# Kernel tuning notes

Measured on AMD Instinct MI355X. Metric: run time of the kernel, lower is better.

The kernel has to match this reference:

```python
import jax, jax.numpy as jnp
import numpy as np

B, A, D = 256, 32, 2048  # batch, num attributes, hidden_dim


def setup_inputs() -> dict:
    key = jax.random.key(0)
    k1, k2, k3, k4, k5 = jax.random.split(key, 5)
    x = jax.random.normal(k1, (B, D), dtype=jnp.float32)
    attribute_feat = jax.random.normal(k2, (B, A, D), dtype=jnp.float32)
    attribute_label = jax.random.randint(k3, (B, A), 0, 2, dtype=jnp.int64)
    # GraphConvolution parameters (glorot-style scale)
    W = jax.random.normal(k4, (D, D), dtype=jnp.float32) * (1.0 / np.sqrt(D))
    b = jnp.zeros((D,), dtype=jnp.float32)
    return {"x": x, "attribute_feat": attribute_feat,
            "attribute_label": attribute_label, "W": W, "b": b}


def reference(x, attribute_feat, attribute_label, W, b):
    # Star adjacency: nonzero attribute nodes <-> global node (index A)
    mask = (attribute_label > 0).astype(x.dtype)            # [B, A]
    adj = jnp.zeros((B, A + 1, A + 1), dtype=x.dtype)
    adj = adj.at[:, :A, A].set(mask).at[:, A, :A].set(mask)  # [B, A+1, A+1]
    # Vertex features: attributes + global node (x) per sample
    vertex = jnp.concatenate([attribute_feat, x[:, None, :]], axis=1)  # [B, A+1, D]
    # GCN layer: tanh(adj @ (vertex @ W) + b); dropout is identity in eval
    support = jnp.einsum('bnd,de->bne', vertex, W)           # [B, A+1, D]
    out = jnp.tanh(jnp.einsum('bnm,bmd->bnd', adj, support) + b)
    # Return updated global-node embedding per sample
    return out[:, -1, :]                                     # [B, D]
```

## Files before the change

kernel.cpp:

```cpp
#include <hip/hip_runtime.h>
#include <hip/hip_bf16.h>

typedef unsigned short ushort_t;
using ushort4v = __attribute__((ext_vector_type(4))) ushort_t;
using ushort8 = __attribute__((ext_vector_type(8))) ushort_t;
using short8  = __attribute__((ext_vector_type(8))) short;
using float4v = __attribute__((ext_vector_type(4))) float;

#define Bsz 256
#define Aattr 32
#define Ddim 2048
#define OUTN (Bsz * Ddim)

__device__ __forceinline__ float bf2f(ushort_t u) {
    union { unsigned int i; float f; } c;
    c.i = ((unsigned int)u) << 16;
    return c.f;
}

__device__ __forceinline__ ushort_t f2bf(float f) {
    union { float f; unsigned int i; } c;
    c.f = f;
    unsigned int x = c.i;
    unsigned int r = (x + 0x7FFFu + ((x >> 16) & 1u)) >> 16;
    return (ushort_t)r;
}

struct BfPair { ushort_t hi, lo; };
__device__ __forceinline__ BfPair split_bf16(float x) {
    BfPair p;
    p.hi = f2bf(x);
    p.lo = f2bf(x - bf2f(p.hi));
    return p;
}

__global__ __launch_bounds__(256) void k_prep(
    const float* __restrict__ feat, const int* __restrict__ label,
    const float* __restrict__ W,
    ushort_t* __restrict__ s_hi, ushort_t* __restrict__ s_lo,
    ushort_t* __restrict__ WT_hi, ushort_t* __restrict__ WT_lo) {
    __shared__ float tile[64][65];
    const int t = threadIdx.x;

    if (blockIdx.x < 512) {
        int* list = (int*)&tile[0][0];
        int* cntp = (int*)&tile[1][0];
        const int b    = blockIdx.x >> 1;
        const int half = blockIdx.x & 1;

        if (t < 64) {
            int lab = label[b * Aattr + (t & 31)];
            unsigned long long vote = __ballot(lab > 0);
            unsigned m32 = (unsigned)(vote & 0xFFFFFFFFull);
            if (t < 32) {
                if (lab > 0) {
                    int rank = __popc(m32 & ((1u << t) - 1u));
                    list[rank] = t;
                }
                if (t == 0) *cntp = __popc(m32);
            }
        }
        __syncthreads();

        const int n  = *cntp;
        const int d0 = half * 1024 + t * 4;
        const float* fb = feat + (size_t)b * (Aattr * Ddim) + d0;

        float a0 = 0.f, a1 = 0.f, a2 = 0.f, a3 = 0.f;
        int i = 0;
        for (; i + 4 <= n; i += 4) {
            const int j0 = list[i], j1 = list[i+1], j2 = list[i+2], j3 = list[i+3];
            float4 v0 = *(const float4*)(fb + j0 * Ddim);
            float4 v1 = *(const float4*)(fb + j1 * Ddim);
            float4 v2 = *(const float4*)(fb + j2 * Ddim);
            float4 v3 = *(const float4*)(fb + j3 * Ddim);
            a0 += v0.x + v1.x + v2.x + v3.x;
            a1 += v0.y + v1.y + v2.y + v3.y;
            a2 += v0.z + v1.z + v2.z + v3.z;
            a3 += v0.w + v1.w + v2.w + v3.w;
        }
        for (; i < n; ++i) {
            float4 v = *(const float4*)(fb + list[i] * Ddim);
            a0 += v.x; a1 += v.y; a2 += v.z; a3 += v.w;
        }

        ushort4v hi, lo;
        BfPair p0 = split_bf16(a0); hi[0] = p0.hi; lo[0] = p0.lo;
        BfPair p1 = split_bf16(a1); hi[1] = p1.hi; lo[1] = p1.lo;
        BfPair p2 = split_bf16(a2); hi[2] = p2.hi; lo[2] = p2.lo;
        BfPair p3 = split_bf16(a3); hi[3] = p3.hi; lo[3] = p3.lo;
        *(ushort4v*)(s_hi + (size_t)b * Ddim + d0) = hi;
        *(ushort4v*)(s_lo + (size_t)b * Ddim + d0) = lo;
    } else {
        const int q  = blockIdx.x - 512;
        const int bx = q & 31;
        const int by = q >> 5;

#pragma unroll
        for (int p = 0; p < 4; ++p) {
            const int row = p * 16 + (t >> 4);
            const int c   = (t & 15) * 4;
            float4 v = *(const float4*)(W + (size_t)(by * 64 + row) * Ddim + bx * 64 + c);
            tile[row][c + 0] = v.x;
            tile[row][c + 1] = v.y;
            tile[row][c + 2] = v.z;
            tile[row][c + 3] = v.w;
        }
        __syncthreads();
#pragma unroll
        for (int p = 0; p < 2; ++p) {
            const int er = p * 32 + (t >> 3);
            const int dc = (t & 7) * 8;
            ushort8 hi, lo;
#pragma unroll
            for (int j = 0; j < 8; ++j) {
                BfPair pr = split_bf16(tile[dc + j][er]);
                hi[j] = pr.hi; lo[j] = pr.lo;
            }
            const size_t off = (size_t)(bx * 64 + er) * Ddim + by * 64 + dc;
            *(ushort8*)(WT_hi + off) = hi;
            *(ushort8*)(WT_lo + off) = lo;
        }
    }
}

__global__ __launch_bounds__(64) void k_gemm(
    const ushort_t* __restrict__ S_hi, const ushort_t* __restrict__ S_lo,
    const ushort_t* __restrict__ WT_hi, const ushort_t* __restrict__ WT_lo,
    float* __restrict__ partials, int KS, int lks, int kchunk) {
    const int g    = blockIdx.x;
    const int ks   = g & (KS - 1);
    const int r    = g >> lks;
    const int m0   = (r & 3) * 64;
    const int n0   = (r >> 2) * 64;
    const int k0   = ks * kchunk;

    const int l    = threadIdx.x;
    const int quad = l >> 4;
    const int m16  = l & 15;

    float4v acc[4][4];
#pragma unroll
    for (int i = 0; i < 4; ++i)
#pragma unroll
        for (int j = 0; j < 4; ++j) acc[i][j] = {0.f, 0.f, 0.f, 0.f};

    const size_t aoff = (size_t)(m0 + m16) * Ddim + quad * 8;
    const size_t boff = (size_t)(n0 + m16) * Ddim + quad * 8;
    const ushort_t* Ah = S_hi + aoff;
    const ushort_t* Al = S_lo + aoff;
    const ushort_t* Bh = WT_hi + boff;
    const ushort_t* Bl = WT_lo + boff;

    for (int k = k0; k < k0 + kchunk; k += 32) {
        short8 ah[4], al[4], bh[4], bl[4];
#pragma unroll
        for (int i = 0; i < 4; ++i) {
            const size_t o = (size_t)(i * 16) * Ddim + k;
            ah[i] = *(const short8*)(Ah + o);
            al[i] = *(const short8*)(Al + o);
            bh[i] = *(const short8*)(Bh + o);
            bl[i] = *(const short8*)(Bl + o);
        }
#pragma unroll
        for (int mi = 0; mi < 4; ++mi) {
#pragma unroll
            for (int ni = 0; ni < 4; ++ni) {
                acc[mi][ni] = __builtin_amdgcn_mfma_f32_16x16x32_bf16(ah[mi], bh[ni], acc[mi][ni], 0, 0, 0);
                acc[mi][ni] = __builtin_amdgcn_mfma_f32_16x16x32_bf16(ah[mi], bl[ni], acc[mi][ni], 0, 0, 0);
                acc[mi][ni] = __builtin_amdgcn_mfma_f32_16x16x32_bf16(al[mi], bh[ni], acc[mi][ni], 0, 0, 0);
            }
        }
    }

    float* pout = partials + (size_t)ks * OUTN;
#pragma unroll
    for (int mi = 0; mi < 4; ++mi) {
#pragma unroll
        for (int ni = 0; ni < 4; ++ni) {
            const int n = n0 + ni * 16 + m16;
#pragma unroll
            for (int rr = 0; rr < 4; ++rr) {
                const int m = m0 + mi * 16 + quad * 4 + rr;
                pout[(size_t)m * Ddim + n] = acc[mi][ni][rr];
            }
        }
    }
}

__global__ __launch_bounds__(256) void k_finish(
    const float* __restrict__ partials, const float* __restrict__ bias,
    float* __restrict__ out, int KS) {
    const int i = (blockIdx.x * 256 + threadIdx.x) * 4;
    float a0 = 0.f, a1 = 0.f, a2 = 0.f, a3 = 0.f;
    for (int s = 0; s < KS; ++s) {
        float4 v = *(const float4*)(partials + (size_t)s * OUTN + i);
        a0 += v.x; a1 += v.y; a2 += v.z; a3 += v.w;
    }
    float4 bv = *(const float4*)(bias + (i & (Ddim - 1)));
    float4 o;
    o.x = tanhf(a0 + bv.x);
    o.y = tanhf(a1 + bv.y);
    o.z = tanhf(a2 + bv.z);
    o.w = tanhf(a3 + bv.w);
    *(float4*)(out + i) = o;
}

extern "C" void kernel_launch(void* const* d_in, const int* in_sizes, int n_in,
                              void* d_out, int out_size, void* d_ws, size_t ws_size,
                              hipStream_t stream) {
    const float* feat  = (const float*)d_in[1];
    const int*   label = (const int*)d_in[2];
    const float* W     = (const float*)d_in[3];
    const float* bias  = (const float*)d_in[4];
    float*       out   = (float*)d_out;

    char* ws = (char*)d_ws;
    ushort_t* s_hi  = (ushort_t*)ws;
    ushort_t* s_lo  = (ushort_t*)(ws + (1u << 20));
    ushort_t* WT_hi = (ushort_t*)(ws + (2u << 20));
    ushort_t* WT_lo = (ushort_t*)(ws + (10u << 20));
    float* partials = (float*)(ws + (18u << 20));

    const size_t avail = ws_size > (18u << 20) ? ws_size - (18u << 20) : 0;
    int KS = 1, lks = 0;
    while (KS < 8 && (size_t)(KS * 2) * (OUTN * sizeof(float)) <= avail) { KS *= 2; ++lks; }
    const int kchunk = Ddim / KS;

    k_prep<<<dim3(1536), dim3(256), 0, stream>>>(feat, label, W, s_hi, s_lo, WT_hi, WT_lo);
    k_gemm<<<dim3(128 * KS), dim3(64), 0, stream>>>(s_hi, s_lo, WT_hi, WT_lo,
                                                    partials, KS, lks, kchunk);
    k_finish<<<dim3(OUTN / 1024), dim3(256), 0, stream>>>(partials, bias, out, KS);
}
```

Baseline: 138.8 us.

## Fuse split-K reduction and tanh epilogue into GEMM via in-block LDS reduction

Replaces the split-K GEMM, which wrote per-split partials to global memory, and the separate finish kernel with one kernel. Each 256-thread block covers a 32x64 output tile, its four waves each take a quarter of K, and the partial sums are reduced through shared memory before bias and tanh are applied in place. This removes a kernel launch and the global round trip of up to 8 partial buffers. In exchange the grid shrinks to 256 blocks with smaller M tiles, which lowers B-operand reuse and may leave compute units underused.

Result: no change. 137.9 us (median of 2 runs) (-0.6%).

```diff
diff --git a/kernel.cpp b/kernel.cpp
--- a/kernel.cpp
+++ b/kernel.cpp
@@ -10,7 +10,6 @@
 #define Bsz 256
 #define Aattr 32
 #define Ddim 2048
-#define OUTN (Bsz * Ddim)
 
 __device__ __forceinline__ float bf2f(ushort_t u) {
     union { unsigned int i; float f; } c;
@@ -124,24 +123,28 @@
     }
 }
 
-__global__ __launch_bounds__(64) void k_gemm(
+__global__ __launch_bounds__(256) void k_gemm2(
     const ushort_t* __restrict__ S_hi, const ushort_t* __restrict__ S_lo,
     const ushort_t* __restrict__ WT_hi, const ushort_t* __restrict__ WT_lo,
-    float* __restrict__ partials, int KS, int lks, int kchunk) {
-    const int g    = blockIdx.x;
-    const int ks   = g & (KS - 1);
-    const int r    = g >> lks;
-    const int m0   = (r & 3) * 64;
-    const int n0   = (r >> 2) * 64;
-    const int k0   = ks * kchunk;
-
-    const int l    = threadIdx.x;
+    const float* __restrict__ bias, float* __restrict__ out) {
+    __shared__ float red[4][32 * 64];
+
+    const int g      = blockIdx.x;
+    const int n_tile = (g & 7) * 4 + (g >> 6);
+    const int m_tile = (g >> 3) & 7;
+    const int m0     = m_tile * 32;
+    const int n0     = n_tile * 64;
+
+    const int t    = threadIdx.x;
+    const int w    = t >> 6;
+    const int l    = t & 63;
     const int quad = l >> 4;
     const int m16  = l & 15;
-
-    float4v acc[4][4];
-#pragma unroll
-    for (int i = 0; i < 4; ++i)
+    const int k0   = w * 512;
+
+    float4v acc[2][4];
+#pragma unroll
+    for (int i = 0; i < 2; ++i)
 #pragma unroll
         for (int j = 0; j < 4; ++j) acc[i][j] = {0.f, 0.f, 0.f, 0.f};
 
@@ -152,58 +155,68 @@
     const ushort_t* Bh = WT_hi + boff;
     const ushort_t* Bl = WT_lo + boff;
 
-    for (int k = k0; k < k0 + kchunk; k += 32) {
-        short8 ah[4], al[4], bh[4], bl[4];
+    for (int k = k0; k < k0 + 512; k += 32) {
+        short8 ah0 = *(const short8*)(Ah + k);
+        short8 ah1 = *(const short8*)(Ah + 16 * Ddim + k);
+        short8 al0 = *(const short8*)(Al + k);
+        short8 al1 = *(const short8*)(Al + 16 * Ddim + k);
+        short8 bh[4], bl[4];
 #pragma unroll
         for (int i = 0; i < 4; ++i) {
             const size_t o = (size_t)(i * 16) * Ddim + k;
-            ah[i] = *(const short8*)(Ah + o);
-            al[i] = *(const short8*)(Al + o);
             bh[i] = *(const short8*)(Bh + o);
             bl[i] = *(const short8*)(Bl + o);
         }
 #pragma unroll
-        for (int mi = 0; mi < 4; ++mi) {
-#pragma unroll
-            for (int ni = 0; ni < 4; ++ni) {
-                acc[mi][ni] = __builtin_amdgcn_mfma_f32_16x16x32_bf16(ah[mi], bh[ni], acc[mi][ni], 0, 0, 0);
-                acc[mi][ni] = __builtin_amdgcn_mfma_f32_16x16x32_bf16(ah[mi], bl[ni], acc[mi][ni], 0, 0, 0);
-                acc[mi][ni] = __builtin_amdgcn_mfma_f32_16x16x32_bf16(al[mi], bh[ni], acc[mi][ni], 0, 0, 0);
+        for (int ni = 0; ni < 4; ++ni) {
+            acc[0][ni] = __builtin_amdgcn_mfma_f32_16x16x32_bf16(ah0, bh[ni], acc[0][ni], 0, 0, 0);
+            acc[0][ni] = __builtin_amdgcn_mfma_f32_16x16x32_bf16(ah0, bl[ni], acc[0][ni], 0, 0, 0);
+            acc[0][ni] = __builtin_amdgcn_mfma_f32_16x16x32_bf16(al0, bh[ni], acc[0][ni], 0, 0, 0);
+            acc[1][ni] = __builtin_amdgcn_mfma_f32_16x16x32_bf16(ah1, bh[ni], acc[1][ni], 0, 0, 0);
+            acc[1][ni] = __builtin_amdgcn_mfma_f32_16x16x32_bf16(ah1, bl[ni], acc[1][ni], 0, 0, 0);
+            acc[1][ni] = __builtin_amdgcn_mfma_f32_16x16x32_bf16(al1, bh[ni], acc[1][ni], 0, 0, 0);
+        }
+    }
+
+#pragma unroll
+    for (int mi = 0; mi < 2; ++mi) {
+#pragma unroll
+        for (int ni = 0; ni < 4; ++ni) {
+#pragma unroll
+            for (int rr = 0; rr < 4; ++rr) {
+                red[w][(mi * 16 + quad * 4 + rr) * 64 + ni * 16 + m16] = acc[mi][ni][rr];
             }
         }
     }
-
-    float* pout = partials + (size_t)ks * OUTN;
-#pragma unroll
-    for (int mi = 0; mi < 4; ++mi) {
-#pragma unroll
-        for (int ni = 0; ni < 4; ++ni) {
-            const int n = n0 + ni * 16 + m16;
-#pragma unroll
-            for (int rr = 0; rr < 4; ++rr) {
-                const int m = m0 + mi * 16 + quad * 4 + rr;
-                pout[(size_t)m * Ddim + n] = acc[mi][ni][rr];
-            }
-        }
-    }
-}
-
-__global__ __launch_bounds__(256) void k_finish(
-    const float* __restrict__ partials, const float* __restrict__ bias,
-    float* __restrict__ out, int KS) {
-    const int i = (blockIdx.x * 256 + threadIdx.x) * 4;
-    float a0 = 0.f, a1 = 0.f, a2 = 0.f, a3 = 0.f;
-    for (int s = 0; s < KS; ++s) {
-        float4 v = *(const float4*)(partials + (size_t)s * OUTN + i);
-        a0 += v.x; a1 += v.y; a2 += v.z; a3 += v.w;
-    }
-    float4 bv = *(const float4*)(bias + (i & (Ddim - 1)));
-    float4 o;
-    o.x = tanhf(a0 + bv.x);
-    o.y = tanhf(a1 + bv.y);
-    o.z = tanhf(a2 + bv.z);
-    o.w = tanhf(a3 + bv.w);
-    *(float4*)(out + i) = o;
+    __syncthreads();
+
+    const int m_l = t >> 3;
+    const int n_l = (t & 7) * 8;
+    const int base = m_l * 64 + n_l;
+    float s[8];
+#pragma unroll
+    for (int j = 0; j < 8; ++j) s[j] = 0.f;
+#pragma unroll
+    for (int ww = 0; ww < 4; ++ww) {
+        float4 v0 = *(const float4*)&red[ww][base];
+        float4 v1 = *(const float4*)&red[ww][base + 4];
+        s[0] += v0.x; s[1] += v0.y; s[2] += v0.z; s[3] += v0.w;
+        s[4] += v1.x; s[5] += v1.y; s[6] += v1.z; s[7] += v1.w;
+    }
+    float4 b0 = *(const float4*)(bias + n0 + n_l);
+    float4 b1 = *(const float4*)(bias + n0 + n_l + 4);
+    float4 o0, o1;
+    o0.x = tanhf(s[0] + b0.x);
+    o0.y = tanhf(s[1] + b0.y);
+    o0.z = tanhf(s[2] + b0.z);
+    o0.w = tanhf(s[3] + b0.w);
+    o1.x = tanhf(s[4] + b1.x);
+    o1.y = tanhf(s[5] + b1.y);
+    o1.z = tanhf(s[6] + b1.z);
+    o1.w = tanhf(s[7] + b1.w);
+    float* op = out + (size_t)(m0 + m_l) * Ddim + n0 + n_l;
+    *(float4*)op = o0;
+    *(float4*)(op + 4) = o1;
 }
 
 extern "C" void kernel_launch(void* const* d_in, const int* in_sizes, int n_in,
@@ -220,15 +233,7 @@
     ushort_t* s_lo  = (ushort_t*)(ws + (1u << 20));
     ushort_t* WT_hi = (ushort_t*)(ws + (2u << 20));
     ushort_t* WT_lo = (ushort_t*)(ws + (10u << 20));
-    float* partials = (float*)(ws + (18u << 20));
-
-    const size_t avail = ws_size > (18u << 20) ? ws_size - (18u << 20) : 0;
-    int KS = 1, lks = 0;
-    while (KS < 8 && (size_t)(KS * 2) * (OUTN * sizeof(float)) <= avail) { KS *= 2; ++lks; }
-    const int kchunk = Ddim / KS;
 
     k_prep<<<dim3(1536), dim3(256), 0, stream>>>(feat, label, W, s_hi, s_lo, WT_hi, WT_lo);
-    k_gemm<<<dim3(128 * KS), dim3(64), 0, stream>>>(s_hi, s_lo, WT_hi, WT_lo,
-                                                    partials, KS, lks, kchunk);
-    k_finish<<<dim3(OUTN / 1024), dim3(256), 0, stream>>>(partials, bias, out, KS);
-}
+    k_gemm2<<<dim3(256), dim3(256), 0, stream>>>(s_hi, s_lo, WT_hi, WT_lo, bias, out);
+}
```

## Fuse split-K reduction and tanh epilogue into GEMM via shared memory

Applied to the files above, without the earlier changes.

The GEMM now uses 256-thread blocks where each of four waves handles a quarter of K, reducing partial tiles in shared memory and applying bias plus tanh directly. This removes the global partials buffer round-trip and the separate finish kernel launch. In exchange the grid shrinks to 128 blocks, fewer than before when KS was 8, and the block tile order is remapped. It also uses 64KB of shared memory per block, which limits occupancy.

After: 147.9 us. 1.07x slower.

```diff
diff --git a/kernel.cpp b/kernel.cpp
--- a/kernel.cpp
+++ b/kernel.cpp
@@ -10,7 +10,6 @@
 #define Bsz 256
 #define Aattr 32
 #define Ddim 2048
-#define OUTN (Bsz * Ddim)
 
 __device__ __forceinline__ float bf2f(ushort_t u) {
     union { unsigned int i; float f; } c;
@@ -124,20 +123,24 @@
     }
 }
 
-__global__ __launch_bounds__(64) void k_gemm(
+__global__ __launch_bounds__(256) void k_gemm2(
     const ushort_t* __restrict__ S_hi, const ushort_t* __restrict__ S_lo,
     const ushort_t* __restrict__ WT_hi, const ushort_t* __restrict__ WT_lo,
-    float* __restrict__ partials, int KS, int lks, int kchunk) {
-    const int g    = blockIdx.x;
-    const int ks   = g & (KS - 1);
-    const int r    = g >> lks;
-    const int m0   = (r & 3) * 64;
-    const int n0   = (r >> 2) * 64;
-    const int k0   = ks * kchunk;
-
-    const int l    = threadIdx.x;
+    const float* __restrict__ bias, float* __restrict__ out) {
+    __shared__ float red[4][64 * 64];
+
+    const int g      = blockIdx.x;
+    const int n_tile = (g & 7) * 4 + (g >> 5);
+    const int m_tile = (g >> 3) & 3;
+    const int m0     = m_tile * 64;
+    const int n0     = n_tile * 64;
+
+    const int t    = threadIdx.x;
+    const int w    = t >> 6;
+    const int l    = t & 63;
     const int quad = l >> 4;
     const int m16  = l & 15;
+    const int k0   = w * 512;
 
     float4v acc[4][4];
 #pragma unroll
@@ -152,7 +155,8 @@
     const ushort_t* Bh = WT_hi + boff;
     const ushort_t* Bl = WT_lo + boff;
 
-    for (int k = k0; k < k0 + kchunk; k += 32) {
+#pragma unroll 2
+    for (int k = k0; k < k0 + 512; k += 32) {
         short8 ah[4], al[4], bh[4], bl[4];
 #pragma unroll
         for (int i = 0; i < 4; ++i) {
@@ -173,37 +177,35 @@
         }
     }
 
-    float* pout = partials + (size_t)ks * OUTN;
 #pragma unroll
     for (int mi = 0; mi < 4; ++mi) {
 #pragma unroll
         for (int ni = 0; ni < 4; ++ni) {
-            const int n = n0 + ni * 16 + m16;
 #pragma unroll
             for (int rr = 0; rr < 4; ++rr) {
-                const int m = m0 + mi * 16 + quad * 4 + rr;
-                pout[(size_t)m * Ddim + n] = acc[mi][ni][rr];
-            }
-        }
-    }
-}
-
-__global__ __launch_bounds__(256) void k_finish(
-    const float* __restrict__ partials, const float* __restrict__ bias,
-    float* __restrict__ out, int KS) {
-    const int i = (blockIdx.x * 256 + threadIdx.x) * 4;
-    float a0 = 0.f, a1 = 0.f, a2 = 0.f, a3 = 0.f;
-    for (int s = 0; s < KS; ++s) {
-        float4 v = *(const float4*)(partials + (size_t)s * OUTN + i);
-        a0 += v.x; a1 += v.y; a2 += v.z; a3 += v.w;
-    }
-    float4 bv = *(const float4*)(bias + (i & (Ddim - 1)));
-    float4 o;
-    o.x = tanhf(a0 + bv.x);
-    o.y = tanhf(a1 + bv.y);
-    o.z = tanhf(a2 + bv.z);
-    o.w = tanhf(a3 + bv.w);
-    *(float4*)(out + i) = o;
+                red[w][(mi * 16 + quad * 4 + rr) * 64 + ni * 16 + m16] = acc[mi][ni][rr];
+            }
+        }
+    }
+    __syncthreads();
+
+    const int c4 = (t & 15) * 4;
+    float4 bv = *(const float4*)(bias + n0 + c4);
+#pragma unroll
+    for (int p = 0; p < 4; ++p) {
+        const int row = p * 16 + (t >> 4);
+        const int idx = row * 64 + c4;
+        float4 v0 = *(const float4*)&red[0][idx];
+        float4 v1 = *(const float4*)&red[1][idx];
+        float4 v2 = *(const float4*)&red[2][idx];
+        float4 v3 = *(const float4*)&red[3][idx];
+        float4 o;
+        o.x = tanhf(v0.x + v1.x + v2.x + v3.x + bv.x);
+        o.y = tanhf(v0.y + v1.y + v2.y + v3.y + bv.y);
+        o.z = tanhf(v0.z + v1.z + v2.z + v3.z + bv.z);
+        o.w = tanhf(v0.w + v1.w + v2.w + v3.w + bv.w);
+        *(float4*)(out + (size_t)(m0 + row) * Ddim + n0 + c4) = o;
+    }
 }
 
 extern "C" void kernel_launch(void* const* d_in, const int* in_sizes, int n_in,
@@ -220,15 +222,7 @@
     ushort_t* s_lo  = (ushort_t*)(ws + (1u << 20));
     ushort_t* WT_hi = (ushort_t*)(ws + (2u << 20));
     ushort_t* WT_lo = (ushort_t*)(ws + (10u << 20));
-    float* partials = (float*)(ws + (18u << 20));
-
-    const size_t avail = ws_size > (18u << 20) ? ws_size - (18u << 20) : 0;
-    int KS = 1, lks = 0;
-    while (KS < 8 && (size_t)(KS * 2) * (OUTN * sizeof(float)) <= avail) { KS *= 2; ++lks; }
-    const int kchunk = Ddim / KS;
 
     k_prep<<<dim3(1536), dim3(256), 0, stream>>>(feat, label, W, s_hi, s_lo, WT_hi, WT_lo);
-    k_gemm<<<dim3(128 * KS), dim3(64), 0, stream>>>(s_hi, s_lo, WT_hi, WT_lo,
-                                                    partials, KS, lks, kchunk);
-    k_finish<<<dim3(OUTN / 1024), dim3(256), 0, stream>>>(partials, bias, out, KS);
-}
+    k_gemm2<<<dim3(128), dim3(256), 0, stream>>>(s_hi, s_lo, WT_hi, WT_lo, bias, out);
+}
```
